# Kernel optimization log

Hardware: AMD Instinct MI355X
Metric: run time of the kernel (lower is better)

Reference implementation:

```python
import jax, jax.numpy as jnp
import numpy as np

# Dims: batch, queries, graph nodes, text len, hidden, heads, layers, ffn
B, NQ, NN, T, D, H, LAYERS, FF = 16, 32, 128, 352, 768, 8, 6, 3072
L = NQ + NN + T          # 512 total sequence length
HD = D // H              # 96 head dim
NEG = -1e9               # additive mask value (HF uses dtype min; -1e9 is equivalent post-softmax)
LN_EPS = 1e-12           # BERT LayerNorm eps


def _ln(x, g, b):
    m = x.mean(-1, keepdims=True)
    v = ((x - m) ** 2).mean(-1, keepdims=True)
    return (x - m) * jax.lax.rsqrt(v + LN_EPS) * g + b


def setup_inputs() -> dict:
    key = jax.random.key(0)
    ks = iter(jax.random.split(key, 32))

    def nrm(shape, s=0.02):
        return jax.random.normal(next(ks), shape, jnp.float32) * s

    return {
        "graph_node_features": jax.random.normal(next(ks), (B, NN, D), jnp.float32),
        "text_embeds": jax.random.normal(next(ks), (B, T, D), jnp.float32),
        "text_atts": jnp.ones((B, T), jnp.int32),
        "graph_mask": jnp.ones((B, NN), jnp.int32),
        "query_tokens": nrm((1, NQ, D), 1.0),   # nn.Parameter(torch.randn(...))
        "gproj_w": nrm((D, D)), "gproj_b": jnp.zeros((D,)),
        "pos_emb": nrm((L, D)), "tok_emb": nrm((D,)),  # token_type row 0
        "emb_ln_g": jnp.ones((D,)), "emb_ln_b": jnp.zeros((D,)),
        "qkv_w": nrm((LAYERS, D, 3 * D)), "qkv_b": jnp.zeros((LAYERS, 3 * D)),
        "ao_w": nrm((LAYERS, D, D)), "ao_b": jnp.zeros((LAYERS, D)),
        "ln1_g": jnp.ones((LAYERS, D)), "ln1_b": jnp.zeros((LAYERS, D)),
        "ff1_w": nrm((LAYERS, D, FF)), "ff1_b": jnp.zeros((LAYERS, FF)),
        "ff2_w": nrm((LAYERS, FF, D)), "ff2_b": jnp.zeros((LAYERS, D)),
        "ln2_g": jnp.ones((LAYERS, D)), "ln2_b": jnp.zeros((LAYERS, D)),
    }


def _itg_bias(text_atts, graph_mask):
    # Build the custom ITG prefix-LM mask: bidirectional over [queries|graph],
    # causal over text, and queries/graph blocked from attending to text.
    keep = jnp.concatenate(
        [jnp.ones((B, NQ), jnp.int32), graph_mask, text_atts], axis=1)  # [B, L]
    ts = NQ + NN
    idx = jnp.arange(L)
    is_text = idx >= ts
    pair = (keep[:, :, None] * keep[:, None, :]).astype(bool)          # padding mask
    causal_ok = jnp.where(is_text[:, None] & is_text[None, :],
                          idx[:, None] >= idx[None, :], True)           # tril in text block
    block_ok = ~((~is_text)[:, None] & is_text[None, :])                # prefix cannot see text
    mask = pair & causal_ok & block_ok                                  # [B, L, L]
    return jnp.where(mask, 0.0, NEG)[:, None, :, :]                     # [B, 1, L, L]


def reference(graph_node_features, text_embeds, text_atts, graph_mask,
              query_tokens, gproj_w, gproj_b, pos_emb, tok_emb,
              emb_ln_g, emb_ln_b, qkv_w, qkv_b, ao_w, ao_b,
              ln1_g, ln1_b, ff1_w, ff1_b, ff2_w, ff2_b, ln2_g, ln2_b):
    gfeat = graph_node_features @ gproj_w + gproj_b
    qtok = jnp.broadcast_to(query_tokens, (B, NQ, D))
    x = jnp.concatenate([qtok, gfeat, text_embeds], axis=1)             # [B, L, D]
    bias = _itg_bias(text_atts, graph_mask)

    # BERT embeddings (inputs_embeds path): + position + token_type(0), LN (dropout off)
    x = _ln(x + pos_emb[None] + tok_emb, emb_ln_g, emb_ln_b)

    scale = 1.0 / np.sqrt(HD)
    for i in range(LAYERS):
        qkv = x @ qkv_w[i] + qkv_b[i]
        q, k, v = jnp.split(qkv, 3, axis=-1)
        q = q.reshape(B, L, H, HD)
        k = k.reshape(B, L, H, HD)
        v = v.reshape(B, L, H, HD)
        s = jnp.einsum('bqhd,bkhd->bhqk', q, k) * scale + bias
        p = jax.nn.softmax(s, axis=-1)
        ctx = jnp.einsum('bhqk,bkhd->bqhd', p, v).reshape(B, L, D)
        x = _ln(x + ctx @ ao_w[i] + ao_b[i], ln1_g[i], ln1_b[i])
        h = jax.nn.gelu(x @ ff1_w[i] + ff1_b[i], approximate=False)
        x = _ln(x + h @ ff2_w[i] + ff2_b[i], ln2_g[i], ln2_b[i])

    return x[:, NQ + NN:, :]   # text_feats [B, T, D]
```

## Files before the change

kernel.cpp:

```cpp
#include <hip/hip_runtime.h>
#include <math.h>

typedef __bf16 bf16;
typedef __bf16 bf16x8 __attribute__((ext_vector_type(8)));
typedef float f32x4 __attribute__((ext_vector_type(4)));

#define NQ   32
#define NN_  128
#define TT   352
#define DD   768
#define NH   8
#define HDIM 96
#define LSEQ 512
#define TSPLIT 160
#define FFD  3072
#define NLAYER 6
#define NBATCH 16

template <int ACT>
__global__ __launch_bounds__(256) void gemm_bt(
    const bf16* __restrict__ A, const bf16* __restrict__ Bt,
    bf16* __restrict__ C, const float* __restrict__ bias,
    int K, int lda, int ldb, int ldc, int zdiv,
    long sA1, long sA2, long sB1, long sB2, long sC1, long sC2,
    float alpha, int Nstore)
{
    __shared__ __attribute__((aligned(16))) bf16 As[128 * 32];
    __shared__ __attribute__((aligned(16))) bf16 Bs[128 * 32];

    const int bz = blockIdx.z;
    const int z1 = bz / zdiv, z2 = bz % zdiv;
    A  += (size_t)z1 * sA1 + (size_t)z2 * sA2;
    Bt += (size_t)z1 * sB1 + (size_t)z2 * sB2;
    C  += (size_t)z1 * sC1 + (size_t)z2 * sC2;

    const int n0 = blockIdx.x * 128, m0 = blockIdx.y * 128;
    const int t = threadIdx.x;
    const int w = t >> 6, l = t & 63;
    const int wm = w >> 1, wn = w & 1;
    const int lr = l & 15, quad = l >> 4;

    f32x4 acc[4][4] = {};

    const int f0 = w * 1024 + l * 8;
    const int ra0 = f0 >> 5, ca0 = f0 & 31;
    const int ra1 = (f0 + 512) >> 5, ca1 = (f0 + 512) & 31;
    bf16* ldsA0 = &As[w * 1024];
    bf16* ldsA1 = &As[w * 1024 + 512];
    bf16* ldsB0 = &Bs[w * 1024];
    bf16* ldsB1 = &Bs[w * 1024 + 512];
    const bf16* a0 = A  + (size_t)(m0 + ra0) * lda + ca0;
    const bf16* a1 = A  + (size_t)(m0 + ra1) * lda + ca1;
    const bf16* b0 = Bt + (size_t)(n0 + ra0) * ldb + ca0;
    const bf16* b1 = Bt + (size_t)(n0 + ra1) * ldb + ca1;

    for (int k0 = 0; k0 < K; k0 += 32) {
        __syncthreads();
        __builtin_amdgcn_global_load_lds(
            (const __attribute__((address_space(1))) void*)(a0 + k0),
            (__attribute__((address_space(3))) void*)ldsA0, 16, 0, 0);
        __builtin_amdgcn_global_load_lds(
            (const __attribute__((address_space(1))) void*)(a1 + k0),
            (__attribute__((address_space(3))) void*)ldsA1, 16, 0, 0);
        __builtin_amdgcn_global_load_lds(
            (const __attribute__((address_space(1))) void*)(b0 + k0),
            (__attribute__((address_space(3))) void*)ldsB0, 16, 0, 0);
        __builtin_amdgcn_global_load_lds(
            (const __attribute__((address_space(1))) void*)(b1 + k0),
            (__attribute__((address_space(3))) void*)ldsB1, 16, 0, 0);
        __syncthreads();

        bf16x8 af[4], bf_[4];
#pragma unroll
        for (int i = 0; i < 4; ++i)
            af[i] = *(const bf16x8*)&As[(wm * 64 + i * 16 + lr) * 32 + quad * 8];
#pragma unroll
        for (int j = 0; j < 4; ++j)
            bf_[j] = *(const bf16x8*)&Bs[(wn * 64 + j * 16 + lr) * 32 + quad * 8];
#pragma unroll
        for (int i = 0; i < 4; ++i)
#pragma unroll
            for (int j = 0; j < 4; ++j)
                acc[i][j] = __builtin_amdgcn_mfma_f32_16x16x32_bf16(af[i], bf_[j], acc[i][j], 0, 0, 0);
    }

#pragma unroll
    for (int i = 0; i < 4; ++i) {
        const int grow = m0 + wm * 64 + i * 16 + quad * 4;
#pragma unroll
        for (int j = 0; j < 4; ++j) {
            const int gcol = n0 + wn * 64 + j * 16 + lr;
            if (gcol >= Nstore) continue;
            float bv = bias ? bias[gcol] : 0.0f;
#pragma unroll
            for (int r = 0; r < 4; ++r) {
                float v = acc[i][j][r] * alpha + bv;
                if (ACT == 1) v = 0.5f * v * (1.0f + erff(v * 0.70710678118654752f));
                C[(size_t)(grow + r) * ldc + gcol] = (bf16)v;
            }
        }
    }
}

__global__ void transpose_w(const float* __restrict__ in, bf16* __restrict__ out,
                            int R, int C)
{
    __shared__ bf16 tile[32][33];
    const int c0 = blockIdx.x * 32, r0 = blockIdx.y * 32;
    const int tx = threadIdx.x & 31, ty = threadIdx.x >> 5;
    for (int i = ty; i < 32; i += 8)
        tile[i][tx] = (bf16)in[(size_t)(r0 + i) * C + c0 + tx];
    __syncthreads();
    for (int i = ty; i < 32; i += 8)
        out[(size_t)(c0 + i) * R + r0 + tx] = tile[tx][i];
}

__global__ void cvt_bf16(const float* __restrict__ in, bf16* __restrict__ out, int n)
{
    const int idx = blockIdx.x * 256 + threadIdx.x;
    if (idx < n) out[idx] = (bf16)in[idx];
}

__global__ void transpose_v(const bf16* __restrict__ qkv, bf16* __restrict__ vT)
{
    __shared__ bf16 tile[32][33];
    const int z = blockIdx.z;
    const int zb = z >> 3, h = z & 7;
    const bf16* src = qkv + (size_t)zb * LSEQ * 2304 + 1536 + h * HDIM;
    bf16* dst = vT + (size_t)z * 128 * LSEQ;
    const int l0 = blockIdx.x * 32, d0 = blockIdx.y * 32;
    const int tx = threadIdx.x & 31, ty = threadIdx.x >> 5;
    for (int i = ty; i < 32; i += 8)
        tile[i][tx] = (d0 + tx < HDIM) ? src[(size_t)(l0 + i) * 2304 + d0 + tx]
                                       : (bf16)0.f;
    __syncthreads();
    for (int i = ty; i < 32; i += 8)
        dst[(size_t)(d0 + i) * LSEQ + l0 + tx] = tile[tx][i];
}

__device__ __forceinline__ void block_reduce_2(float& a, float& b)
{
#pragma unroll
    for (int off = 32; off; off >>= 1) {
        a += __shfl_xor(a, off);
        b += __shfl_xor(b, off);
    }
    __shared__ float sa[4], sb[4];
    const int w = threadIdx.x >> 6;
    if ((threadIdx.x & 63) == 0) { sa[w] = a; sb[w] = b; }
    __syncthreads();
    a = sa[0] + sa[1] + sa[2] + sa[3];
    b = sb[0] + sb[1] + sb[2] + sb[3];
}

__global__ void embed_ln(const float* __restrict__ qtok, const bf16* __restrict__ gfeat,
                         const float* __restrict__ text, const float* __restrict__ pos,
                         const float* __restrict__ tok, const float* __restrict__ g,
                         const float* __restrict__ bb, bf16* __restrict__ x)
{
    const int row = blockIdx.x;
    const int l = row & 511, b = row >> 9;
    const int t = threadIdx.x;

    float vals[3], s = 0.f, sq = 0.f;
#pragma unroll
    for (int c = 0; c < 3; ++c) {
        const int d = t + c * 256;
        float base;
        if (l < NQ)           base = qtok[(size_t)l * DD + d];
        else if (l < TSPLIT)  base = (float)gfeat[((size_t)b * NN_ + (l - NQ)) * DD + d];
        else                  base = text[((size_t)b * TT + (l - TSPLIT)) * DD + d];
        float v = base + pos[(size_t)l * DD + d] + tok[d];
        vals[c] = v; s += v; sq += v * v;
    }
    block_reduce_2(s, sq);
    const float mean = s * (1.f / 768.f);
    const float var = sq * (1.f / 768.f) - mean * mean;
    const float rs = rsqrtf(var + 1e-12f);
    bf16* o = x + (size_t)row * DD;
#pragma unroll
    for (int c = 0; c < 3; ++c) {
        const int d = t + c * 256;
        o[d] = (bf16)((vals[c] - mean) * rs * g[d] + bb[d]);
    }
}

__global__ void ln_rows(const bf16* __restrict__ X, const bf16* __restrict__ Y,
                        bf16* __restrict__ Out, const float* __restrict__ g,
                        const float* __restrict__ bb)
{
    const int row = blockIdx.x;
    const int t = threadIdx.x;
    const bf16* xr = X + (size_t)row * DD;
    const bf16* yr = Y + (size_t)row * DD;
    float vals[3], s = 0.f, sq = 0.f;
#pragma unroll
    for (int c = 0; c < 3; ++c) {
        const int d = t + c * 256;
        float v = (float)xr[d] + (float)yr[d];
        vals[c] = v; s += v; sq += v * v;
    }
    block_reduce_2(s, sq);
    const float mean = s * (1.f / 768.f);
    const float var = sq * (1.f / 768.f) - mean * mean;
    const float rs = rsqrtf(var + 1e-12f);
    bf16* o = Out + (size_t)row * DD;
#pragma unroll
    for (int c = 0; c < 3; ++c) {
        const int d = t + c * 256;
        o[d] = (bf16)((vals[c] - mean) * rs * g[d] + bb[d]);
    }
}

__global__ void softmax_mask(bf16* __restrict__ S, const int* __restrict__ tatts,
                             const int* __restrict__ gmask, int b0)
{
    const int wid = blockIdx.x * 4 + (threadIdx.x >> 6);
    const int lane = threadIdx.x & 63;
    const int i = wid & 511;
    const int bh = wid >> 9;
    const int b = b0 + (bh >> 3);
    bf16* p = S + (size_t)wid * 512;

    const int keep_i = (i < NQ) ? 1 : (i < TSPLIT ? gmask[b * NN_ + i - NQ]
                                                  : tatts[b * TT + i - TSPLIT]);
    float v[8];
    float m = -INFINITY;
#pragma unroll
    for (int c = 0; c < 8; ++c) {
        const int j = c * 64 + lane;
        const int keep_j = (j < NQ) ? 1 : (j < TSPLIT ? gmask[b * NN_ + j - NQ]
                                                      : tatts[b * TT + j - TSPLIT]);
        bool ok = keep_i && keep_j;
        if (i < TSPLIT && j >= TSPLIT) ok = false;
        if (i >= TSPLIT && j >= TSPLIT && i < j) ok = false;
        float s = (float)p[j] + (ok ? 0.f : -1e9f);
        v[c] = s;
        m = fmaxf(m, s);
    }
#pragma unroll
    for (int off = 32; off; off >>= 1) m = fmaxf(m, __shfl_xor(m, off));
    float sum = 0.f;
#pragma unroll
    for (int c = 0; c < 8; ++c) { v[c] = __expf(v[c] - m); sum += v[c]; }
#pragma unroll
    for (int off = 32; off; off >>= 1) sum += __shfl_xor(sum, off);
    const float inv = 1.f / sum;
#pragma unroll
    for (int c = 0; c < 8; ++c) p[c * 64 + lane] = (bf16)(v[c] * inv);
}

__global__ void copy_out(const bf16* __restrict__ x, float* __restrict__ out)
{
    const size_t idx = (size_t)blockIdx.x * 256 + threadIdx.x;
    const int d = idx % DD;
    const size_t row = idx / DD;
    const int t = row % TT;
    const int b = row / TT;
    out[idx] = (float)x[((size_t)b * LSEQ + TSPLIT + t) * DD + d];
}

static void launch_gemm(const bf16* A, const bf16* Bt, bf16* C, const float* bias,
                        int M, int K, int lda, int ldb, int ldc,
                        int batches, int zdiv,
                        long sA1, long sA2, long sB1, long sB2, long sC1, long sC2,
                        float alpha, int Nstore, int act, hipStream_t stream)
{
    dim3 grid((Nstore + 127) / 128, M / 128, batches);
    if (act)
        gemm_bt<1><<<grid, 256, 0, stream>>>(A, Bt, C, bias, K, lda, ldb, ldc, zdiv,
                                             sA1, sA2, sB1, sB2, sC1, sC2, alpha, Nstore);
    else
        gemm_bt<0><<<grid, 256, 0, stream>>>(A, Bt, C, bias, K, lda, ldb, ldc, zdiv,
                                             sA1, sA2, sB1, sB2, sC1, sC2, alpha, Nstore);
}

extern "C" void kernel_launch(void* const* d_in, const int* in_sizes, int n_in,
                              void* d_out, int out_size, void* d_ws, size_t ws_size,
                              hipStream_t stream)
{
    const float* gnf     = (const float*)d_in[0];
    const float* text    = (const float*)d_in[1];
    const int*   tatts   = (const int*)d_in[2];
    const int*   gmask   = (const int*)d_in[3];
    const float* qtok    = (const float*)d_in[4];
    const float* gproj_w = (const float*)d_in[5];
    const float* gproj_b = (const float*)d_in[6];
    const float* pos     = (const float*)d_in[7];
    const float* tok     = (const float*)d_in[8];
    const float* eg      = (const float*)d_in[9];
    const float* eb      = (const float*)d_in[10];
    const float* qkv_w   = (const float*)d_in[11];
    const float* qkv_b   = (const float*)d_in[12];
    const float* ao_w    = (const float*)d_in[13];
    const float* ao_b    = (const float*)d_in[14];
    const float* ln1g    = (const float*)d_in[15];
    const float* ln1b    = (const float*)d_in[16];
    const float* ff1_w   = (const float*)d_in[17];
    const float* ff1_b   = (const float*)d_in[18];
    const float* ff2_w   = (const float*)d_in[19];
    const float* ff2_b   = (const float*)d_in[20];
    const float* ln2g    = (const float*)d_in[21];
    const float* ln2b    = (const float*)d_in[22];
    float* out = (float*)d_out;

    const bool big = ws_size >= (size_t)169000000;
    const int CB = big ? 16 : 4;
    const int NC = NBATCH / CB;
    const int FC = big ? 1 : 2;
    const int FM = 8192 / FC;

    bf16* ws = (bf16*)d_ws;
    size_t off = 0;
    auto alloc = [&](size_t n) { bf16* p = ws + off; off += n; return p; };
    bf16* wt1  = alloc(2359296);
    bf16* wt2  = alloc(2359296);
    bf16* x    = alloc(6291456);
    bf16* qkvb = alloc((size_t)CB * 512 * 2304);
    bf16* ctx  = alloc(6291456);
    bf16* t1   = alloc(6291456);
    bf16* u    = alloc(big ? 41943040 : 12582912);
    bf16* vTc  = u;
    bf16* Sc   = u + (size_t)CB * 524288;
    bf16* hbuf = u;
    bf16* gfeat = t1;
    bf16* gnfb  = qkvb;

    dim3 blk(256);

    cvt_bf16<<<6144, blk, 0, stream>>>(gnf, gnfb, 1572864);
    transpose_w<<<dim3(24, 24), blk, 0, stream>>>(gproj_w, wt1, 768, 768);
    launch_gemm(gnfb, wt1, gfeat, gproj_b, 2048, 768, 768, 768, 768,
                1, 1, 0, 0, 0, 0, 0, 0, 1.f, 768, 0, stream);
    embed_ln<<<8192, blk, 0, stream>>>(qtok, gfeat, text, pos, tok, eg, eb, x);

    const float scale = 0.10206207261596577f;
    for (int i = 0; i < NLAYER; ++i) {
        transpose_w<<<dim3(72, 24), blk, 0, stream>>>(
            qkv_w + (size_t)i * 768 * 2304, wt1, 768, 2304);
        for (int c = 0; c < NC; ++c) {
            launch_gemm(x + (size_t)c * CB * 512 * 768, wt1, qkvb, qkv_b + i * 2304,
                        CB * 512, 768, 768, 768, 2304, 1, 1, 0, 0, 0, 0, 0, 0,
                        1.f, 2304, 0, stream);
            transpose_v<<<dim3(16, 4, CB * 8), blk, 0, stream>>>(qkvb, vTc);
            launch_gemm(qkvb, qkvb + 768, Sc, nullptr, 512, 96, 2304, 2304, 512,
                        CB * 8, 8, 1179648, 96, 1179648, 96, 2097152, 262144,
                        scale, 512, 0, stream);
            softmax_mask<<<CB * 1024, blk, 0, stream>>>(Sc, tatts, gmask, c * CB);
            launch_gemm(Sc, vTc, ctx + (size_t)c * CB * 512 * 768, nullptr,
                        512, 512, 512, 512, 768,
                        CB * 8, 8, 2097152, 262144, 524288, 65536, 393216, 96,
                        1.f, 96, 0, stream);
        }
        transpose_w<<<dim3(24, 24), blk, 0, stream>>>(
            ao_w + (size_t)i * 589824, wt1, 768, 768);
        launch_gemm(ctx, wt1, t1, ao_b + i * 768, 8192, 768, 768, 768, 768,
                    1, 1, 0, 0, 0, 0, 0, 0, 1.f, 768, 0, stream);
        ln_rows<<<8192, blk, 0, stream>>>(x, t1, x, ln1g + i * 768, ln1b + i * 768);

        transpose_w<<<dim3(96, 24), blk, 0, stream>>>(
            ff1_w + (size_t)i * 2359296, wt1, 768, 3072);
        transpose_w<<<dim3(24, 96), blk, 0, stream>>>(
            ff2_w + (size_t)i * 2359296, wt2, 3072, 768);
        for (int c = 0; c < FC; ++c) {
            launch_gemm(x + (size_t)c * FM * 768, wt1, hbuf, ff1_b + i * 3072,
                        FM, 768, 768, 768, 3072, 1, 1, 0, 0, 0, 0, 0, 0,
                        1.f, 3072, 1, stream);
            launch_gemm(hbuf, wt2, t1 + (size_t)c * FM * 768, ff2_b + i * 768,
                        FM, 3072, 3072, 3072, 768, 1, 1, 0, 0, 0, 0, 0, 0,
                        1.f, 768, 0, stream);
        }
        ln_rows<<<8192, blk, 0, stream>>>(x, t1, x, ln2g + i * 768, ln2b + i * 768);
    }

    copy_out<<<16896, blk, 0, stream>>>(x, out);

    (void)in_sizes; (void)n_in; (void)out_size;
}
```

Before: 2.447 ms.

## Fuse attention into a flash-attention kernel that skips fully masked key tiles

```diff
diff --git a/kernel.cpp b/kernel.cpp
--- a/kernel.cpp
+++ b/kernel.cpp
@@ -21,18 +21,10 @@
 __global__ __launch_bounds__(256) void gemm_bt(
     const bf16* __restrict__ A, const bf16* __restrict__ Bt,
     bf16* __restrict__ C, const float* __restrict__ bias,
-    int K, int lda, int ldb, int ldc, int zdiv,
-    long sA1, long sA2, long sB1, long sB2, long sC1, long sC2,
-    float alpha, int Nstore)
+    int K, int lda, int ldb, int ldc, float alpha, int Nstore)
 {
     __shared__ __attribute__((aligned(16))) bf16 As[128 * 32];
     __shared__ __attribute__((aligned(16))) bf16 Bs[128 * 32];
-
-    const int bz = blockIdx.z;
-    const int z1 = bz / zdiv, z2 = bz % zdiv;
-    A  += (size_t)z1 * sA1 + (size_t)z2 * sA2;
-    Bt += (size_t)z1 * sB1 + (size_t)z2 * sB2;
-    C  += (size_t)z1 * sC1 + (size_t)z2 * sC2;
 
     const int n0 = blockIdx.x * 128, m0 = blockIdx.y * 128;
     const int t = threadIdx.x;
@@ -102,6 +94,161 @@
     }
 }
 
+__global__ __launch_bounds__(256) void flash_attn(
+    const bf16* __restrict__ qkv, bf16* __restrict__ ctx,
+    const int* __restrict__ tatts, const int* __restrict__ gmask)
+{
+    __shared__ __attribute__((aligned(16))) bf16 Qs[64 * 104];
+    __shared__ __attribute__((aligned(16))) bf16 Ks[64 * 104];
+    __shared__ __attribute__((aligned(16))) bf16 Vs[96 * 72];
+    __shared__ __attribute__((aligned(16))) bf16 Ps[64 * 72];
+    __shared__ int keep[512];
+
+    const int qt = blockIdx.x;
+    const int bh = blockIdx.y;
+    const int b = bh >> 3, h = bh & 7;
+    const int q0 = qt * 64;
+    const int t = threadIdx.x;
+    const int w = t >> 6, l = t & 63;
+    const int lr = l & 15, quad = l >> 4;
+    const float scale = 0.10206207261596577f;
+
+    const bf16* qbase = qkv + (size_t)b * 512 * 2304 + h * 96;
+    const bf16* kbase = qbase + 768;
+    const bf16* vbase = qbase + 1536;
+
+    for (int j = t; j < 512; j += 256)
+        keep[j] = (j < NQ) ? 1 : (j < TSPLIT ? gmask[b * NN_ + j - NQ]
+                                             : tatts[b * TT + j - TSPLIT]);
+
+#pragma unroll
+    for (int c = 0; c < 3; ++c) {
+        const int idx = t * 8 + c * 2048;
+        const int r = idx / 96, d = idx % 96;
+        *(bf16x8*)&Qs[r * 104 + d] =
+            *(const bf16x8*)&qbase[(size_t)(q0 + r) * 2304 + d];
+    }
+    __syncthreads();
+
+    int ki[4];
+    int ig[4];
+#pragma unroll
+    for (int r = 0; r < 4; ++r) {
+        ig[r] = q0 + w * 16 + quad * 4 + r;
+        ki[r] = keep[ig[r]];
+    }
+
+    float m_run[4] = {-1e30f, -1e30f, -1e30f, -1e30f};
+    float l_run[4] = {0.f, 0.f, 0.f, 0.f};
+    f32x4 oc[6] = {};
+
+    const int JMAX = (qt < 3) ? 128 : q0;
+    for (int j0 = 0; j0 <= JMAX; j0 += 64) {
+        __syncthreads();
+#pragma unroll
+        for (int c = 0; c < 3; ++c) {
+            const int idx = t * 8 + c * 2048;
+            const int r = idx / 96, d = idx % 96;
+            *(bf16x8*)&Ks[r * 104 + d] =
+                *(const bf16x8*)&kbase[(size_t)(j0 + r) * 2304 + d];
+            bf16x8 vv = *(const bf16x8*)&vbase[(size_t)(j0 + r) * 2304 + d];
+#pragma unroll
+            for (int jj = 0; jj < 8; ++jj)
+                Vs[(d + jj) * 72 + r] = vv[jj];
+        }
+        __syncthreads();
+
+        bf16x8 aq[3];
+#pragma unroll
+        for (int ds = 0; ds < 3; ++ds)
+            aq[ds] = *(const bf16x8*)&Qs[(w * 16 + lr) * 104 + ds * 32 + quad * 8];
+        f32x4 sc[4];
+#pragma unroll
+        for (int cb = 0; cb < 4; ++cb) {
+            f32x4 a = {};
+#pragma unroll
+            for (int ds = 0; ds < 3; ++ds) {
+                bf16x8 bk = *(const bf16x8*)&Ks[(cb * 16 + lr) * 104 + ds * 32 + quad * 8];
+                a = __builtin_amdgcn_mfma_f32_16x16x32_bf16(aq[ds], bk, a, 0, 0, 0);
+            }
+            sc[cb] = a;
+        }
+
+        float tm[4] = {-1e30f, -1e30f, -1e30f, -1e30f};
+#pragma unroll
+        for (int cb = 0; cb < 4; ++cb) {
+            const int jg = j0 + cb * 16 + lr;
+            const int kj = keep[jg];
+#pragma unroll
+            for (int r = 0; r < 4; ++r) {
+                const int i = ig[r];
+                bool ok = ki[r] && kj;
+                if (i < TSPLIT && jg >= TSPLIT) ok = false;
+                if (i >= TSPLIT && jg >= TSPLIT && i < jg) ok = false;
+                float s = sc[cb][r] * scale + (ok ? 0.f : -1e9f);
+                sc[cb][r] = s;
+                tm[r] = fmaxf(tm[r], s);
+            }
+        }
+#pragma unroll
+        for (int off = 1; off < 16; off <<= 1)
+#pragma unroll
+            for (int r = 0; r < 4; ++r)
+                tm[r] = fmaxf(tm[r], __shfl_xor(tm[r], off));
+
+        float alpha_[4], ts[4] = {0.f, 0.f, 0.f, 0.f};
+#pragma unroll
+        for (int r = 0; r < 4; ++r) {
+            const float mn = fmaxf(m_run[r], tm[r]);
+            alpha_[r] = __expf(m_run[r] - mn);
+            m_run[r] = mn;
+            l_run[r] *= alpha_[r];
+        }
+#pragma unroll
+        for (int db = 0; db < 6; ++db)
+#pragma unroll
+            for (int r = 0; r < 4; ++r)
+                oc[db][r] *= alpha_[r];
+
+#pragma unroll
+        for (int cb = 0; cb < 4; ++cb)
+#pragma unroll
+            for (int r = 0; r < 4; ++r) {
+                const float p = __expf(sc[cb][r] - m_run[r]);
+                ts[r] += p;
+                Ps[(w * 16 + quad * 4 + r) * 72 + cb * 16 + lr] = (bf16)p;
+            }
+#pragma unroll
+        for (int off = 1; off < 16; off <<= 1)
+#pragma unroll
+            for (int r = 0; r < 4; ++r)
+                ts[r] += __shfl_xor(ts[r], off);
+#pragma unroll
+        for (int r = 0; r < 4; ++r) l_run[r] += ts[r];
+
+        __syncthreads();
+
+#pragma unroll
+        for (int l0 = 0; l0 < 64; l0 += 32) {
+            bf16x8 ap = *(const bf16x8*)&Ps[(w * 16 + lr) * 72 + l0 + quad * 8];
+#pragma unroll
+            for (int db = 0; db < 6; ++db) {
+                bf16x8 bv = *(const bf16x8*)&Vs[(db * 16 + lr) * 72 + l0 + quad * 8];
+                oc[db] = __builtin_amdgcn_mfma_f32_16x16x32_bf16(ap, bv, oc[db], 0, 0, 0);
+            }
+        }
+    }
+
+#pragma unroll
+    for (int r = 0; r < 4; ++r) {
+        const float inv = 1.f / l_run[r];
+        bf16* orow = ctx + ((size_t)b * 512 + ig[r]) * 768 + h * 96;
+#pragma unroll
+        for (int db = 0; db < 6; ++db)
+            orow[db * 16 + lr] = (bf16)(oc[db][r] * inv);
+    }
+}
+
 __global__ void transpose_w(const float* __restrict__ in, bf16* __restrict__ out,
                             int R, int C)
 {
@@ -121,23 +268,6 @@
     if (idx < n) out[idx] = (bf16)in[idx];
 }
 
-__global__ void transpose_v(const bf16* __restrict__ qkv, bf16* __restrict__ vT)
-{
-    __shared__ bf16 tile[32][33];
-    const int z = blockIdx.z;
-    const int zb = z >> 3, h = z & 7;
-    const bf16* src = qkv + (size_t)zb * LSEQ * 2304 + 1536 + h * HDIM;
-    bf16* dst = vT + (size_t)z * 128 * LSEQ;
-    const int l0 = blockIdx.x * 32, d0 = blockIdx.y * 32;
-    const int tx = threadIdx.x & 31, ty = threadIdx.x >> 5;
-    for (int i = ty; i < 32; i += 8)
-        tile[i][tx] = (d0 + tx < HDIM) ? src[(size_t)(l0 + i) * 2304 + d0 + tx]
-                                       : (bf16)0.f;
-    __syncthreads();
-    for (int i = ty; i < 32; i += 8)
-        dst[(size_t)(d0 + i) * LSEQ + l0 + tx] = tile[tx][i];
-}
-
 __device__ __forceinline__ void block_reduce_2(float& a, float& b)
 {
 #pragma unroll
@@ -212,44 +342,6 @@
     }
 }
 
-__global__ void softmax_mask(bf16* __restrict__ S, const int* __restrict__ tatts,
-                             const int* __restrict__ gmask, int b0)
-{
-    const int wid = blockIdx.x * 4 + (threadIdx.x >> 6);
-    const int lane = threadIdx.x & 63;
-    const int i = wid & 511;
-    const int bh = wid >> 9;
-    const int b = b0 + (bh >> 3);
-    bf16* p = S + (size_t)wid * 512;
-
-    const int keep_i = (i < NQ) ? 1 : (i < TSPLIT ? gmask[b * NN_ + i - NQ]
-                                                  : tatts[b * TT + i - TSPLIT]);
-    float v[8];
-    float m = -INFINITY;
-#pragma unroll
-    for (int c = 0; c < 8; ++c) {
-        const int j = c * 64 + lane;
-        const int keep_j = (j < NQ) ? 1 : (j < TSPLIT ? gmask[b * NN_ + j - NQ]
-                                                      : tatts[b * TT + j - TSPLIT]);
-        bool ok = keep_i && keep_j;
-        if (i < TSPLIT && j >= TSPLIT) ok = false;
-        if (i >= TSPLIT && j >= TSPLIT && i < j) ok = false;
-        float s = (float)p[j] + (ok ? 0.f : -1e9f);
-        v[c] = s;
-        m = fmaxf(m, s);
-    }
-#pragma unroll
-    for (int off = 32; off; off >>= 1) m = fmaxf(m, __shfl_xor(m, off));
-    float sum = 0.f;
-#pragma unroll
-    for (int c = 0; c < 8; ++c) { v[c] = __expf(v[c] - m); sum += v[c]; }
-#pragma unroll
-    for (int off = 32; off; off >>= 1) sum += __shfl_xor(sum, off);
-    const float inv = 1.f / sum;
-#pragma unroll
-    for (int c = 0; c < 8; ++c) p[c * 64 + lane] = (bf16)(v[c] * inv);
-}
-
 __global__ void copy_out(const bf16* __restrict__ x, float* __restrict__ out)
 {
     const size_t idx = (size_t)blockIdx.x * 256 + threadIdx.x;
@@ -262,17 +354,13 @@
 
 static void launch_gemm(const bf16* A, const bf16* Bt, bf16* C, const float* bias,
                         int M, int K, int lda, int ldb, int ldc,
-                        int batches, int zdiv,
-                        long sA1, long sA2, long sB1, long sB2, long sC1, long sC2,
                         float alpha, int Nstore, int act, hipStream_t stream)
 {
-    dim3 grid((Nstore + 127) / 128, M / 128, batches);
+    dim3 grid((Nstore + 127) / 128, M / 128, 1);
     if (act)
-        gemm_bt<1><<<grid, 256, 0, stream>>>(A, Bt, C, bias, K, lda, ldb, ldc, zdiv,
-                                             sA1, sA2, sB1, sB2, sC1, sC2, alpha, Nstore);
+        gemm_bt<1><<<grid, 256, 0, stream>>>(A, Bt, C, bias, K, lda, ldb, ldc, alpha, Nstore);
     else
-        gemm_bt<0><<<grid, 256, 0, stream>>>(A, Bt, C, bias, K, lda, ldb, ldc, zdiv,
-                                             sA1, sA2, sB1, sB2, sC1, sC2, alpha, Nstore);
+        gemm_bt<0><<<grid, 256, 0, stream>>>(A, Bt, C, bias, K, lda, ldb, ldc, alpha, Nstore);
 }
 
 extern "C" void kernel_launch(void* const* d_in, const int* in_sizes, int n_in,
@@ -304,76 +392,50 @@
     const float* ln2b    = (const float*)d_in[22];
     float* out = (float*)d_out;
 
-    const bool big = ws_size >= (size_t)169000000;
-    const int CB = big ? 16 : 4;
-    const int NC = NBATCH / CB;
-    const int FC = big ? 1 : 2;
-    const int FM = 8192 / FC;
-
-    bf16* ws = (bf16*)d_ws;
-    size_t off = 0;
-    auto alloc = [&](size_t n) { bf16* p = ws + off; off += n; return p; };
-    bf16* wt1  = alloc(2359296);
-    bf16* wt2  = alloc(2359296);
-    bf16* x    = alloc(6291456);
-    bf16* qkvb = alloc((size_t)CB * 512 * 2304);
-    bf16* ctx  = alloc(6291456);
-    bf16* t1   = alloc(6291456);
-    bf16* u    = alloc(big ? 41943040 : 12582912);
-    bf16* vTc  = u;
-    bf16* Sc   = u + (size_t)CB * 524288;
+    bf16* ws   = (bf16*)d_ws;
+    bf16* wt1  = ws;
+    bf16* wt2  = wt1 + 2359296;
+    bf16* x    = wt2 + 2359296;
+    bf16* ctx  = x   + 6291456;
+    bf16* t1   = ctx + 6291456;
+    bf16* u    = t1  + 6291456;
+    bf16* qkvb = u;
     bf16* hbuf = u;
     bf16* gfeat = t1;
-    bf16* gnfb  = qkvb;
+    bf16* gnfb  = u;
 
     dim3 blk(256);
 
     cvt_bf16<<<6144, blk, 0, stream>>>(gnf, gnfb, 1572864);
     transpose_w<<<dim3(24, 24), blk, 0, stream>>>(gproj_w, wt1, 768, 768);
     launch_gemm(gnfb, wt1, gfeat, gproj_b, 2048, 768, 768, 768, 768,
-                1, 1, 0, 0, 0, 0, 0, 0, 1.f, 768, 0, stream);
+                1.f, 768, 0, stream);
     embed_ln<<<8192, blk, 0, stream>>>(qtok, gfeat, text, pos, tok, eg, eb, x);
 
-    const float scale = 0.10206207261596577f;
     for (int i = 0; i < NLAYER; ++i) {
         transpose_w<<<dim3(72, 24), blk, 0, stream>>>(
             qkv_w + (size_t)i * 768 * 2304, wt1, 768, 2304);
-        for (int c = 0; c < NC; ++c) {
-            launch_gemm(x + (size_t)c * CB * 512 * 768, wt1, qkvb, qkv_b + i * 2304,
-                        CB * 512, 768, 768, 768, 2304, 1, 1, 0, 0, 0, 0, 0, 0,
-                        1.f, 2304, 0, stream);
-            transpose_v<<<dim3(16, 4, CB * 8), blk, 0, stream>>>(qkvb, vTc);
-            launch_gemm(qkvb, qkvb + 768, Sc, nullptr, 512, 96, 2304, 2304, 512,
-                        CB * 8, 8, 1179648, 96, 1179648, 96, 2097152, 262144,
-                        scale, 512, 0, stream);
-            softmax_mask<<<CB * 1024, blk, 0, stream>>>(Sc, tatts, gmask, c * CB);
-            launch_gemm(Sc, vTc, ctx + (size_t)c * CB * 512 * 768, nullptr,
-                        512, 512, 512, 512, 768,
-                        CB * 8, 8, 2097152, 262144, 524288, 65536, 393216, 96,
-                        1.f, 96, 0, stream);
-        }
+        launch_gemm(x, wt1, qkvb, qkv_b + i * 2304,
+                    8192, 768, 768, 768, 2304, 1.f, 2304, 0, stream);
+        flash_attn<<<dim3(8, 128), blk, 0, stream>>>(qkvb, ctx, tatts, gmask);
         transpose_w<<<dim3(24, 24), blk, 0, stream>>>(
             ao_w + (size_t)i * 589824, wt1, 768, 768);
-        launch_gemm(ctx, wt1, t1, ao_b + i * 768, 8192, 768, 768, 768, 768,
-                    1, 1, 0, 0, 0, 0, 0, 0, 1.f, 768, 0, stream);
+        launch_gemm(ctx, wt1, t1, ao_b + i * 768,
+                    8192, 768, 768, 768, 768, 1.f, 768, 0, stream);
         ln_rows<<<8192, blk, 0, stream>>>(x, t1, x, ln1g + i * 768, ln1b + i * 768);
 
         transpose_w<<<dim3(96, 24), blk, 0, stream>>>(
             ff1_w + (size_t)i * 2359296, wt1, 768, 3072);
         transpose_w<<<dim3(24, 96), blk, 0, stream>>>(
             ff2_w + (size_t)i * 2359296, wt2, 3072, 768);
-        for (int c = 0; c < FC; ++c) {
-            launch_gemm(x + (size_t)c * FM * 768, wt1, hbuf, ff1_b + i * 3072,
-                        FM, 768, 768, 768, 3072, 1, 1, 0, 0, 0, 0, 0, 0,
-                        1.f, 3072, 1, stream);
-            launch_gemm(hbuf, wt2, t1 + (size_t)c * FM * 768, ff2_b + i * 768,
-                        FM, 3072, 3072, 3072, 768, 1, 1, 0, 0, 0, 0, 0, 0,
-                        1.f, 768, 0, stream);
-        }
+        launch_gemm(x, wt1, hbuf, ff1_b + i * 3072,
+                    8192, 768, 768, 768, 3072, 1.f, 3072, 1, stream);
+        launch_gemm(hbuf, wt2, t1, ff2_b + i * 768,
+                    8192, 3072, 3072, 3072, 768, 1.f, 768, 0, stream);
         ln_rows<<<8192, blk, 0, stream>>>(x, t1, x, ln2g + i * 768, ln2b + i * 768);
     }
 
     copy_out<<<16896, blk, 0, stream>>>(x, out);
 
-    (void)in_sizes; (void)n_in; (void)out_size;
-}
+    (void)in_sizes; (void)n_in; (void)out_size; (void)ws_size;
+}
```

After: 2.293 ms. -6.3%, faster.
